# Performance work log

Hardware: AMD Instinct MI355X
Metric: run time of the kernel (lower is better)

Reference implementation:

```python
import jax, jax.numpy as jnp
import numpy as np

SCALE = 16.0
IGNORE_THRES = 0.5
NUM_CLASSES = 40
ANCHORS_PX = np.array([[16., 16.], [32., 32.], [64., 64.], [32., 64.], [64., 32.]], dtype=np.float32)
NB, NA, NH, NW, MAXT = 16, 5, 96, 96, 50


def setup_inputs() -> dict:
    key = jax.random.key(0)
    k1, k2, k3, k4, k5, k6, k7 = jax.random.split(key, 7)
    prediction = jax.random.normal(k1, (NB, NA, NH, NW, 5 + NUM_CLASSES), jnp.float32)
    # GT boxes in pixel space; x in [0, NW*SCALE), y in [0, NH*SCALE)
    xs = jax.random.uniform(k2, (NB, MAXT), minval=0.5, maxval=NW - 0.5) * SCALE
    ys = jax.random.uniform(k3, (NB, MAXT), minval=0.5, maxval=NH - 0.5) * SCALE
    hs = jax.random.uniform(k4, (NB, MAXT), minval=0.5, maxval=6.0) * SCALE
    ws = jax.random.uniform(k5, (NB, MAXT), minval=0.5, maxval=6.0) * SCALE
    lbl = jax.random.randint(k6, (NB, MAXT), 0, NUM_CLASSES)
    target = jnp.zeros((NB, MAXT, 13 + NUM_CLASSES), jnp.float32)
    target = target.at[..., 0].set(xs).at[..., 1].set(ys)
    target = target.at[..., 3].set(hs).at[..., 4].set(ws)  # source reads h from col 3, w from col 4
    target = target.at[..., 13:].set(jax.nn.one_hot(lbl, NUM_CLASSES, dtype=jnp.float32))
    target_sizes = jax.random.randint(k7, (NB,), 20, MAXT + 1)
    return {"prediction": prediction, "target": target, "target_sizes": target_sizes}


def _iou_xywh(g, p):
    # center/size boxes -> corners, with the original's +1 pixel convention
    g_x1, g_x2 = g[0] - g[2] / 2, g[0] + g[2] / 2
    g_y1, g_y2 = g[1] - g[3] / 2, g[1] + g[3] / 2
    p_x1, p_x2 = p[0] - p[2] / 2, p[0] + p[2] / 2
    p_y1, p_y2 = p[1] - p[3] / 2, p[1] + p[3] / 2
    iw = jnp.clip(jnp.minimum(g_x2, p_x2) - jnp.maximum(g_x1, p_x1) + 1., 0.)
    ih = jnp.clip(jnp.minimum(g_y2, p_y2) - jnp.maximum(g_y1, p_y1) + 1., 0.)
    inter = iw * ih
    ga = (g_x2 - g_x1 + 1.) * (g_y2 - g_y1 + 1.)
    pa = (p_x2 - p_x1 + 1.) * (p_y2 - p_y1 + 1.)
    return inter / (ga + pa - inter + 1e-16)


def _build_targets(pred_boxes, pred_conf, pred_cls, target, target_sizes, anchors):
    # Sequential scan over (batch, gt) preserves the torch double-loop's
    nB, nA, nH, nW = pred_conf.shape
    maxT = target.shape[1]
    aw, ah = anchors[:, 0], anchors[:, 1]
    anch_area = (aw + 1.) * (ah + 1.)
    mask = jnp.zeros((nB, nA, nH, nW), jnp.float32)
    conf_mask = jnp.ones((nB, nA, nH, nW), jnp.float32)
    tx = jnp.zeros_like(mask); ty = jnp.zeros_like(mask)
    tw = jnp.zeros_like(mask); th = jnp.zeros_like(mask)
    tconf = jnp.zeros_like(mask)
    tlabel = jnp.zeros((nB, nA, nH, nW), jnp.int32)  # argmax of one-hot tcls

    def step(carry, bt):
        mask, conf_mask, tx, ty, tw, th, tconf, tlabel, nGT, nCorrect = carry
        b = bt // maxT
        t = bt % maxT
        valid = t < target_sizes[b]
        row = target[b, t]
        gx = row[0] / SCALE; gy = row[1] / SCALE
        gw = row[4] / SCALE; gh = row[3] / SCALE  # w from col 4, h from col 3 (as in source)
        gi = gx.astype(jnp.int32); gj = gy.astype(jnp.int32)
        # anchor IoU: both boxes anchored at origin, corner-style with +1 (x1y1x2y2=True path)
        inter = jnp.clip(jnp.minimum(gw, aw) + 1., 0.) * jnp.clip(jnp.minimum(gh, ah) + 1., 0.)
        anch_ious = inter / ((gw + 1.) * (gh + 1.) + anch_area - inter + 1e-16)
        bd = jnp.where(valid, b, nB)  # out-of-bounds batch index -> scatter dropped when padded
        cur = conf_mask[b, :, gj, gi]
        conf_mask = conf_mask.at[bd, :, gj, gi].set(jnp.where(anch_ious > IGNORE_THRES, 0., cur), mode='drop')
        best_n = jnp.argmax(anch_ious)
        mask = mask.at[bd, best_n, gj, gi].set(1., mode='drop')
        conf_mask = conf_mask.at[bd, best_n, gj, gi].set(1., mode='drop')
        tx = tx.at[bd, best_n, gj, gi].set(gx - gi.astype(jnp.float32), mode='drop')
        ty = ty.at[bd, best_n, gj, gi].set(gy - gj.astype(jnp.float32), mode='drop')
        tw = tw.at[bd, best_n, gj, gi].set(jnp.log(gw / aw[best_n] + 1e-16), mode='drop')
        th = th.at[bd, best_n, gj, gi].set(jnp.log(gh / ah[best_n] + 1e-16), mode='drop')
        lbl = jnp.argmax(row[13:]).astype(jnp.int32)
        tlabel = tlabel.at[bd, best_n, gj, gi].set(lbl, mode='drop')
        tconf = tconf.at[bd, best_n, gj, gi].set(1., mode='drop')
        iou = _iou_xywh(jnp.stack([gx, gy, gw, gh]), pred_boxes[b, best_n, gj, gi])
        correct = valid & (iou > 0.5) & (jnp.argmax(pred_cls[b, best_n, gj, gi]) == lbl) & (pred_conf[b, best_n, gj, gi] > 0.5)
        return (mask, conf_mask, tx, ty, tw, th, tconf, tlabel,
                nGT + valid.astype(jnp.int32), nCorrect + correct.astype(jnp.int32)), None

    init = (mask, conf_mask, tx, ty, tw, th, tconf, tlabel,
            jnp.array(0, jnp.int32), jnp.array(0, jnp.int32))
    (mask, conf_mask, tx, ty, tw, th, tconf, tlabel, nGT, nCorrect), _ = jax.lax.scan(
        step, init, jnp.arange(nB * maxT))
    return mask, conf_mask, tx, ty, tw, th, tconf, tlabel, nGT, nCorrect


def _yolo_loss(prediction, target, target_sizes):
    nB, nA, nH, nW = prediction.shape[:4]
    pred_conf = prediction[..., 0]
    x = prediction[..., 1]; y = prediction[..., 2]
    h = prediction[..., 3]; w = prediction[..., 4]
    pred_cls = prediction[..., 5:]
    grid_x = jnp.arange(nW, dtype=jnp.float32).reshape(1, 1, 1, nW)
    grid_y = jnp.arange(nH, dtype=jnp.float32).reshape(1, 1, nH, 1)
    anchors = jnp.asarray(ANCHORS_PX) / SCALE  # grid units
    aw = anchors[:, 0].reshape(1, nA, 1, 1)
    ah = anchors[:, 1].reshape(1, nA, 1, 1)
    pred_boxes = jnp.stack([
        x + grid_x, y + grid_y, jnp.exp(w) * aw * jnp.ones_like(w), jnp.exp(h) * ah * jnp.ones_like(h)
    ], axis=-1)
    sg = jax.lax.stop_gradient  # torch uses .cpu().data inside build_targets
    mask, conf_mask, tx, ty, tw, th, tconf, tlabel, nGT, nCorrect = _build_targets(
        sg(pred_boxes), sg(pred_conf), sg(pred_cls), target, target_sizes, anchors)
    nM = jnp.sum(mask)
    mmean = lambda v: jnp.sum(mask * v) / nM  # masked MSE mean (size_average=True)
    loss_x = mmean((x - tx) ** 2)
    loss_y = mmean((y - ty) ** 2)
    loss_w = mmean((w - tw) ** 2)
    loss_h = mmean((h - th) ** 2)
    # BCEWithLogits, numerically stable
    bce = jnp.maximum(pred_conf, 0.) - pred_conf * tconf + jnp.log1p(jnp.exp(-jnp.abs(pred_conf)))
    # torch: conf_mask_false = (conf_mask - mask) as byte used as boolean mask -> nonzero selects
    cmf = (conf_mask != mask).astype(jnp.float32)
    loss_conf = jnp.sum(cmf * bce) / jnp.sum(cmf) + jnp.sum(mask * bce) / nM
    logp = jax.nn.log_softmax(pred_cls, axis=-1)
    ce = -jnp.take_along_axis(logp, tlabel[..., None], axis=-1)[..., 0]
    loss_cls = (1.0 / nB) * jnp.sum(mask * ce) / nM
    loss = loss_x + loss_y + loss_w + loss_h + loss_conf + loss_cls
    nProposals = jnp.sum(pred_conf > 0).astype(jnp.float32)
    recall = nCorrect.astype(jnp.float32) / jnp.maximum(nGT, 1).astype(jnp.float32)
    precision = jnp.where(nProposals > 0, nCorrect.astype(jnp.float32) / jnp.maximum(nProposals, 1.), 1.0)
    return (loss, loss_x + loss_y + loss_w + loss_h, loss_conf, loss_cls, recall, precision)


def reference(prediction, target, target_sizes):
    return _yolo_loss(prediction, target, target_sizes)
```

## Files before the change

kernel.cpp:

```cpp
#include <hip/hip_runtime.h>
#include <math.h>

#define NB 16
#define NA 5
#define NH 96
#define NW 96
#define MAXT 50
#define NC 40
#define CH 45
#define TGT_W 53
#define NCELL (NH*NW)
#define NTOT (NB*NA*NH*NW)
#define IGNORE_THRES 0.5f

#define CONFB 675
#define THREADS_CONF (CONFB*1024)

__device__ __constant__ float c_AW[5] = {1.f, 2.f, 4.f, 2.f, 4.f};
__device__ __constant__ float c_AH[5] = {1.f, 2.f, 4.f, 4.f, 2.f};


__device__ __forceinline__ float softplusf(float p) {
    return fmaxf(p, 0.f) + log1pf(expf(-fabsf(p)));
}

__global__ __launch_bounds__(1024) void fused(
    const float* __restrict__ pred, const float* __restrict__ tgt,
    const int* __restrict__ tsz, double* acc, int* corG, int* propI) {

    __shared__ int   s_key[MAXT], s_best[MAXT], s_ign[MAXT], s_lbl[MAXT];
    __shared__ float s_fx[MAXT], s_fy[MAXT], s_gw[MAXT], s_gh[MAXT];
    __shared__ int   s_cor[MAXT];
    __shared__ int   s_sl[MAXT * NA][6];
    __shared__ double red[16][9];
    __shared__ float sb[16];
    __shared__ int   sp[16];

    const int wave = threadIdx.x >> 6, lane = threadIdx.x & 63;

    if (blockIdx.x >= 16) {
        const int cb = blockIdx.x - 16;
        const unsigned q0 = (unsigned)cb * 1024u + threadIdx.x;
        const unsigned j  = q0 % 45u;
        const bool match  = (j == 0u) || (j == 11u) || (j == 22u) || (j == 33u);
        const int  e      = (int)(j / 11u);
        const float4* __restrict__ p4 = (const float4*)pred;

        float bce = 0.f; int prop = 0;
        unsigned q = q0;
        #pragma unroll 4
        for (int it = 0; it < 12; ++it, q += (unsigned)THREADS_CONF) {
            float4 v = p4[q];
            if (match) {
                float p = (e == 0) ? v.x : ((e == 1) ? v.y : ((e == 2) ? v.z : v.w));
                bce  += softplusf(p);
                prop += (p > 0.f) ? 1 : 0;
            }
        }
        #pragma unroll
        for (int off = 32; off; off >>= 1) {
            bce  += __shfl_down(bce, off);
            prop += __shfl_down(prop, off);
        }
        if (lane == 0) { sb[wave] = bce; sp[wave] = prop; }
        __syncthreads();
        if (threadIdx.x == 0) {
            float tb = 0.f; int tp = 0;
            #pragma unroll
            for (int w2 = 0; w2 < 16; ++w2) { tb += sb[w2]; tp += sp[w2]; }
            atomicAdd(&acc[0], (double)tb);
            atomicAdd(propI, tp);
        }
        return;
    }

    const int b = blockIdx.x;
    const int size_b = tsz[b];

    for (int t = wave; t < MAXT; t += 16) {
        const bool valid = t < size_b;
        const float* row = tgt + ((size_t)b * MAXT + t) * TGT_W;
        const float inv_s = 0.0625f;
        float gx = row[0] * inv_s, gy = row[1] * inv_s;
        float gh_ = row[3] * inv_s, gw_ = row[4] * inv_s;
        int gi = (int)gx, gj = (int)gy;

        float lv = (lane < NC) ? row[13 + lane] : -1e30f;
        int   li = (lane < NC) ? lane : (1 << 30);
        #pragma unroll
        for (int off = 32; off; off >>= 1) {
            float ov = __shfl_xor(lv, off);
            int   oi = __shfl_xor(li, off);
            if (ov > lv || (ov == lv && oi < li)) { lv = ov; li = oi; }
        }
        int lbl = li;

        float best_iou = -1e30f; int best = 0; int ign = 0;
        #pragma unroll
        for (int a = 0; a < 5; ++a) {
            float iw = fmaxf(fminf(gw_, c_AW[a]) + 1.f, 0.f);
            float ih = fmaxf(fminf(gh_, c_AH[a]) + 1.f, 0.f);
            float inter = iw * ih;
            float iou = inter / ((gw_ + 1.f) * (gh_ + 1.f) +
                                 (c_AW[a] + 1.f) * (c_AH[a] + 1.f) - inter + 1e-16f);
            if (iou > IGNORE_THRES) ign |= (1 << a);
            if (iou > best_iou) { best_iou = iou; best = a; }
        }

        size_t pbase = ((((size_t)b * NA + best) * NH + gj) * NW + gi) * CH;
        float pv = (lane < CH) ? pred[pbase + lane] : -1e30f;
        float pc = __shfl(pv, 0);
        float px = __shfl(pv, 1) + (float)gi;
        float py = __shfl(pv, 2) + (float)gj;
        float ph = expf(__shfl(pv, 3)) * c_AH[best];
        float pw = expf(__shfl(pv, 4)) * c_AW[best];

        float gx1 = gx - gw_ * 0.5f, gx2 = gx + gw_ * 0.5f;
        float gy1 = gy - gh_ * 0.5f, gy2 = gy + gh_ * 0.5f;
        float px1 = px - pw * 0.5f, px2 = px + pw * 0.5f;
        float py1 = py - ph * 0.5f, py2 = py + ph * 0.5f;
        float iw2 = fmaxf(fminf(gx2, px2) - fmaxf(gx1, px1) + 1.f, 0.f);
        float ih2 = fmaxf(fminf(gy2, py2) - fmaxf(gy1, py1) + 1.f, 0.f);
        float inter2 = iw2 * ih2;
        float ga = (gx2 - gx1 + 1.f) * (gy2 - gy1 + 1.f);
        float pa = (px2 - px1 + 1.f) * (py2 - py1 + 1.f);
        float iou2 = inter2 / (ga + pa - inter2 + 1e-16f);

        float cv = (lane >= 5 && lane < CH) ? pv : -1e30f;
        int   ci = (lane >= 5 && lane < CH) ? (lane - 5) : (1 << 30);
        #pragma unroll
        for (int off = 32; off; off >>= 1) {
            float ov = __shfl_xor(cv, off);
            int   oi = __shfl_xor(ci, off);
            if (ov > cv || (ov == cv && oi < ci)) { cv = ov; ci = oi; }
        }
        bool correct = valid && (iou2 > 0.5f) && (ci == lbl) && (pc > 0.5f);

        if (lane == 0) {
            s_key[t] = valid ? (gj * NW + gi) : -1;
            s_best[t] = best; s_ign[t] = ign; s_lbl[t] = lbl;
            s_fx[t] = gx - (float)gi; s_fy[t] = gy - (float)gj;
            s_gw[t] = gw_; s_gh[t] = gh_;
            s_cor[t] = correct ? 1 : 0;
        }
    }
    __syncthreads();

    if (threadIdx.x == 0) {
        int c = 0;
        for (int t = 0; t < MAXT; ++t) c += s_cor[t];
        corG[b] = c;
    }

    {
        const int t = threadIdx.x;
        if (t < MAXT) {
            const int myKey = s_key[t];
            bool owner = (myKey >= 0);
            if (owner)
                for (int u = t + 1; u < MAXT; ++u)
                    if (s_key[u] == myKey) { owner = false; break; }

            if (!owner) {
                #pragma unroll
                for (int a = 0; a < 5; ++a) s_sl[t * 5 + a][0] = 0;
            } else {
                int cm = 0x1F, m = 0;
                int w_[5] = {-1, -1, -1, -1, -1};
                for (int u = 0; u < MAXT; ++u) {
                    if (s_key[u] != myKey) continue;
                    cm &= ~s_ign[u];
                    int bn = s_best[u];
                    cm |= (1 << bn); m |= (1 << bn);
                    w_[bn] = u;
                }
                #pragma unroll
                for (int a = 0; a < 5; ++a) {
                    int* eSl = s_sl[t * 5 + a];
                    int ca = (b * NA + a) * NCELL + myKey;
                    int ma = (m >> a) & 1, cma = (cm >> a) & 1;
                    eSl[0] = ca | (ma << 20) | (cma << 21) | (1 << 22);
                    if (ma) {
                        int u = w_[a];
                        eSl[1] = s_lbl[u];
                        eSl[2] = __float_as_int(s_fx[u]);
                        eSl[3] = __float_as_int(s_fy[u]);
                        eSl[4] = __float_as_int(logf(s_gw[u] / c_AW[a] + 1e-16f));
                        eSl[5] = __float_as_int(logf(s_gh[u] / c_AH[a] + 1e-16f));
                    }
                }
            }
        }
    }
    __syncthreads();

    double loc[9];
    #pragma unroll
    for (int c = 0; c < 9; ++c) loc[c] = 0.0;

    for (int s = wave; s < MAXT * NA; s += 16) {
        int flags = s_sl[s][0];
        if (!(flags & (1 << 22))) continue;
        int ca = flags & 0xFFFFF;
        int ma = (flags >> 20) & 1, cma = (flags >> 21) & 1;
        size_t base = (size_t)ca * CH;
        float v = (lane < CH) ? pred[base + lane] : -1e30f;
        float p = __shfl(v, 0);
        float s0 = softplusf(p);
        int cmf = (cma != ma) ? 1 : 0;
        loc[0] += (cmf ? (double)(s0 - p * (float)ma) : 0.0) - (double)s0;
        loc[1] += (double)(cmf - 1);
        if (ma) {
            loc[2] += (double)(s0 - p);
            loc[8] += 1.0;
            float x = __shfl(v, 1), y = __shfl(v, 2);
            float hh = __shfl(v, 3), wv = __shfl(v, 4);
            float fx = __int_as_float(s_sl[s][2]), fy = __int_as_float(s_sl[s][3]);
            float tw_ = __int_as_float(s_sl[s][4]), th_ = __int_as_float(s_sl[s][5]);
            int lbl = s_sl[s][1];
            loc[4] += (double)((x - fx) * (x - fx));
            loc[5] += (double)((y - fy) * (y - fy));
            loc[6] += (double)((wv - tw_) * (wv - tw_));
            loc[7] += (double)((hh - th_) * (hh - th_));
            float cvv = (lane >= 5 && lane < CH) ? v : -1e30f;
            float mx = cvv;
            #pragma unroll
            for (int off = 32; off; off >>= 1) mx = fmaxf(mx, __shfl_xor(mx, off));
            float ex = (lane >= 5 && lane < CH) ? expf(v - mx) : 0.f;
            #pragma unroll
            for (int off = 32; off; off >>= 1) ex += __shfl_xor(ex, off);
            float cll = __shfl(v, 5 + lbl);
            loc[3] += (double)(logf(ex) + mx - cll);
        }
    }

    if (lane == 0) {
        #pragma unroll
        for (int c = 0; c < 9; ++c) red[wave][c] = loc[c];
    }
    __syncthreads();
    if (threadIdx.x < 9) {
        double sum = 0.0;
        #pragma unroll
        for (int w2 = 0; w2 < 16; ++w2) sum += red[w2][threadIdx.x];
        if (sum != 0.0) atomicAdd(&acc[1 + threadIdx.x], sum);
    }
}

__global__ __launch_bounds__(64) void finalize(
    const double* __restrict__ acc, const int* __restrict__ corG,
    const int* __restrict__ tsz, const int* __restrict__ propI, float* out) {
    if (threadIdx.x != 0) return;
    int nCor = 0, nGT = 0;
    for (int b = 0; b < NB; ++b) { nCor += corG[b]; nGT += tsz[b]; }
    int nProp = *propI;

    double nM = acc[9];
    double inv_nM = 1.0 / (nM > 0.0 ? nM : 1e-16);
    double l_coord = (acc[5] + acc[6] + acc[7] + acc[8]) * inv_nM;
    double sum_cmf = (double)NTOT + acc[2];
    double l_conf = (acc[0] + acc[1]) / sum_cmf + acc[3] * inv_nM;
    double l_cls = (1.0 / (double)NB) * acc[4] * inv_nM;
    double loss = l_coord + l_conf + l_cls;
    float recall = (float)nCor / (float)(nGT > 1 ? nGT : 1);
    float precision = (nProp > 0) ? ((float)nCor / fmaxf((float)nProp, 1.f)) : 1.f;
    out[0] = (float)loss;
    out[1] = (float)l_coord;
    out[2] = (float)l_conf;
    out[3] = (float)l_cls;
    out[4] = recall;
    out[5] = precision;
}

extern "C" void kernel_launch(void* const* d_in, const int* in_sizes, int n_in,
                              void* d_out, int out_size, void* d_ws, size_t ws_size,
                              hipStream_t stream) {
    const float* pred = (const float*)d_in[0];
    const float* tgt  = (const float*)d_in[1];
    const int*   tsz  = (const int*)d_in[2];
    float* out = (float*)d_out;

    double* acc = (double*)d_ws;
    int* corG   = (int*)((char*)d_ws + 80);
    int* propI  = (int*)((char*)d_ws + 144);

    hipMemsetAsync(d_ws, 0, 160, stream);
    fused<<<16 + CONFB, 1024, 0, stream>>>(pred, tgt, tsz, acc, corG, propI);
    finalize<<<1, 64, 0, stream>>>(acc, corG, tsz, propI, out);
}
```

Baseline: 202.6 us.

## Replace global atomics and memset with per-block partials, use 512-thread blocks

Per-block sums are now written to dedicated workspace slots instead of being accumulated with global double and int atomics. The finalize kernel reduces those partials in parallel, which removes the memset launch. Blocks shrink from 1024 to 512 threads with more blocks and iterations, and prediction loads use nontemporal hints. The per-batch target blocks now run with only 8 waves, so their serial per-target work spreads over fewer waves. corG must still be fully written by the kernel now that nothing zeroes it.

Measured after the change: 226.0 us. +11.5%, slower.

```diff
diff --git a/kernel.cpp b/kernel.cpp
--- a/kernel.cpp
+++ b/kernel.cpp
@@ -13,46 +13,54 @@
 #define NTOT (NB*NA*NH*NW)
 #define IGNORE_THRES 0.5f
 
-#define CONFB 675
-#define THREADS_CONF (CONFB*1024)
+#define CONFB 900
+#define THREADS_CONF (CONFB*512)
+#define CONF_ITERS 18
+
+typedef float fvec4 __attribute__((ext_vector_type(4)));
 
 __device__ __constant__ float c_AW[5] = {1.f, 2.f, 4.f, 2.f, 4.f};
 __device__ __constant__ float c_AH[5] = {1.f, 2.f, 4.f, 4.f, 2.f};
 
+#define WS_TACC      0
+#define WS_PARTIAL_D 1152
+#define WS_CORG      8352
+#define WS_PARTIAL_I 8416
 
 __device__ __forceinline__ float softplusf(float p) {
     return fmaxf(p, 0.f) + log1pf(expf(-fabsf(p)));
 }
 
-__global__ __launch_bounds__(1024) void fused(
+__global__ __launch_bounds__(512) void fused(
     const float* __restrict__ pred, const float* __restrict__ tgt,
-    const int* __restrict__ tsz, double* acc, int* corG, int* propI) {
+    const int* __restrict__ tsz, double* tacc, double* partial_d,
+    int* corG, int* partial_i) {
 
     __shared__ int   s_key[MAXT], s_best[MAXT], s_ign[MAXT], s_lbl[MAXT];
     __shared__ float s_fx[MAXT], s_fy[MAXT], s_gw[MAXT], s_gh[MAXT];
     __shared__ int   s_cor[MAXT];
     __shared__ int   s_sl[MAXT * NA][6];
-    __shared__ double red[16][9];
-    __shared__ float sb[16];
-    __shared__ int   sp[16];
+    __shared__ double red[8][9];
+    __shared__ float sb[8];
+    __shared__ int   sp[8];
 
     const int wave = threadIdx.x >> 6, lane = threadIdx.x & 63;
 
     if (blockIdx.x >= 16) {
         const int cb = blockIdx.x - 16;
-        const unsigned q0 = (unsigned)cb * 1024u + threadIdx.x;
+        const unsigned q0 = (unsigned)cb * 512u + threadIdx.x;
         const unsigned j  = q0 % 45u;
         const bool match  = (j == 0u) || (j == 11u) || (j == 22u) || (j == 33u);
         const int  e      = (int)(j / 11u);
-        const float4* __restrict__ p4 = (const float4*)pred;
+        const fvec4* __restrict__ p4 = (const fvec4*)pred;
 
         float bce = 0.f; int prop = 0;
         unsigned q = q0;
-        #pragma unroll 4
-        for (int it = 0; it < 12; ++it, q += (unsigned)THREADS_CONF) {
-            float4 v = p4[q];
+        #pragma unroll 6
+        for (int it = 0; it < CONF_ITERS; ++it, q += (unsigned)THREADS_CONF) {
+            fvec4 v = __builtin_nontemporal_load(&p4[q]);
             if (match) {
-                float p = (e == 0) ? v.x : ((e == 1) ? v.y : ((e == 2) ? v.z : v.w));
+                float p = v[e];
                 bce  += softplusf(p);
                 prop += (p > 0.f) ? 1 : 0;
             }
@@ -67,9 +75,9 @@
         if (threadIdx.x == 0) {
             float tb = 0.f; int tp = 0;
             #pragma unroll
-            for (int w2 = 0; w2 < 16; ++w2) { tb += sb[w2]; tp += sp[w2]; }
-            atomicAdd(&acc[0], (double)tb);
-            atomicAdd(propI, tp);
+            for (int w2 = 0; w2 < 8; ++w2) { tb += sb[w2]; tp += sp[w2]; }
+            partial_d[cb] = (double)tb;
+            partial_i[cb] = tp;
         }
         return;
     }
@@ -77,7 +85,7 @@
     const int b = blockIdx.x;
     const int size_b = tsz[b];
 
-    for (int t = wave; t < MAXT; t += 16) {
+    for (int t = wave; t < MAXT; t += 8) {
         const bool valid = t < size_b;
         const float* row = tgt + ((size_t)b * MAXT + t) * TGT_W;
         const float inv_s = 0.0625f;
@@ -198,7 +206,7 @@
     #pragma unroll
     for (int c = 0; c < 9; ++c) loc[c] = 0.0;
 
-    for (int s = wave; s < MAXT * NA; s += 16) {
+    for (int s = wave; s < MAXT * NA; s += 8) {
         int flags = s_sl[s][0];
         if (!(flags & (1 << 22))) continue;
         int ca = flags & 0xFFFFF;
@@ -242,25 +250,47 @@
     if (threadIdx.x < 9) {
         double sum = 0.0;
         #pragma unroll
-        for (int w2 = 0; w2 < 16; ++w2) sum += red[w2][threadIdx.x];
-        if (sum != 0.0) atomicAdd(&acc[1 + threadIdx.x], sum);
+        for (int w2 = 0; w2 < 8; ++w2) sum += red[w2][threadIdx.x];
+        tacc[b * 9 + threadIdx.x] = sum;
     }
 }
 
-__global__ __launch_bounds__(64) void finalize(
-    const double* __restrict__ acc, const int* __restrict__ corG,
-    const int* __restrict__ tsz, const int* __restrict__ propI, float* out) {
+__global__ __launch_bounds__(256) void finalize(
+    const double* __restrict__ tacc, const double* __restrict__ partial_d,
+    const int* __restrict__ corG, const int* __restrict__ partial_i,
+    const int* __restrict__ tsz, float* out) {
+    __shared__ double sd[256];
+    __shared__ int    si[256];
+    double db = 0.0; int ip = 0;
+    for (int i = threadIdx.x; i < CONFB; i += 256) { db += partial_d[i]; ip += partial_i[i]; }
+    sd[threadIdx.x] = db; si[threadIdx.x] = ip;
+    __syncthreads();
+    for (int off = 128; off; off >>= 1) {
+        if (threadIdx.x < off) {
+            sd[threadIdx.x] += sd[threadIdx.x + off];
+            si[threadIdx.x] += si[threadIdx.x + off];
+        }
+        __syncthreads();
+    }
     if (threadIdx.x != 0) return;
+    double sum_bce0 = sd[0];
+    int nProp = si[0];
+
+    double A[9];
+    for (int c = 0; c < 9; ++c) {
+        double s = 0.0;
+        for (int b = 0; b < NB; ++b) s += tacc[b * 9 + c];
+        A[c] = s;
+    }
     int nCor = 0, nGT = 0;
     for (int b = 0; b < NB; ++b) { nCor += corG[b]; nGT += tsz[b]; }
-    int nProp = *propI;
-
-    double nM = acc[9];
+
+    double nM = A[8];
     double inv_nM = 1.0 / (nM > 0.0 ? nM : 1e-16);
-    double l_coord = (acc[5] + acc[6] + acc[7] + acc[8]) * inv_nM;
-    double sum_cmf = (double)NTOT + acc[2];
-    double l_conf = (acc[0] + acc[1]) / sum_cmf + acc[3] * inv_nM;
-    double l_cls = (1.0 / (double)NB) * acc[4] * inv_nM;
+    double l_coord = (A[4] + A[5] + A[6] + A[7]) * inv_nM;
+    double sum_cmf = (double)NTOT + A[1];
+    double l_conf = (sum_bce0 + A[0]) / sum_cmf + A[2] * inv_nM;
+    double l_cls = (1.0 / (double)NB) * A[3] * inv_nM;
     double loss = l_coord + l_conf + l_cls;
     float recall = (float)nCor / (float)(nGT > 1 ? nGT : 1);
     float precision = (nProp > 0) ? ((float)nCor / fmaxf((float)nProp, 1.f)) : 1.f;
@@ -280,11 +310,11 @@
     const int*   tsz  = (const int*)d_in[2];
     float* out = (float*)d_out;
 
-    double* acc = (double*)d_ws;
-    int* corG   = (int*)((char*)d_ws + 80);
-    int* propI  = (int*)((char*)d_ws + 144);
-
-    hipMemsetAsync(d_ws, 0, 160, stream);
-    fused<<<16 + CONFB, 1024, 0, stream>>>(pred, tgt, tsz, acc, corG, propI);
-    finalize<<<1, 64, 0, stream>>>(acc, corG, tsz, propI, out);
+    double* tacc      = (double*)((char*)d_ws + WS_TACC);
+    double* partial_d = (double*)((char*)d_ws + WS_PARTIAL_D);
+    int*    corG      = (int*)((char*)d_ws + WS_CORG);
+    int*    partial_i = (int*)((char*)d_ws + WS_PARTIAL_I);
+
+    fused<<<16 + CONFB, 512, 0, stream>>>(pred, tgt, tsz, tacc, partial_d, corG, partial_i);
+    finalize<<<1, 256, 0, stream>>>(tacc, partial_d, corG, partial_i, tsz, out);
 }
```
